# Performance work log

Measured on AMD Instinct MI355X. Metric: run time of the kernel, lower is better.

The kernel has to match this reference:

```python
import jax, jax.numpy as jnp
import numpy as np

REFRACTORY_PERIOD = 5
DAMPENING_FACTOR = 0.3


def setup_inputs() -> dict:
    key = jax.random.key(0)
    B, T, N = 32, 4096, 256
    x = jax.random.normal(key, (B, T, N), dtype=jnp.float32)
    return {"x": x}


def _refractory_scan(x):
    # x: [B, T, N]; scan over time keeping refractory counter q resident.
    B, T, N = x.shape
    xt = jnp.swapaxes(x, 0, 1)  # [T, B, N]

    def step(q, x_t):
        cond = (x_t > 0) & (q == 0)
        z_t = jnp.where(cond, jnp.ones_like(q), jnp.zeros_like(q))
        q = jnp.maximum(jnp.zeros_like(q), q - 1) + REFRACTORY_PERIOD * z_t
        return q, z_t

    q0 = jnp.zeros((B, N), dtype=x.dtype)
    # Note: the t=0 case in the original (z0 = x0>0, q = R*z0) is exactly the
    # first step of this scan starting from q0 = 0.
    _, z = jax.lax.scan(step, q0, xt)
    return jnp.swapaxes(z, 0, 1)  # [B, T, N]


def reference(x) -> jnp.ndarray:
    # Forward value is exactly z_forward (the surrogate-gradient straight-through
    # construction leaves the value unchanged).
    return _refractory_scan(x)
```

## Files before the change

### kernel.cpp

```cpp
#include <hip/hip_runtime.h>
#include <cstdint>
#include <cstddef>

#define BB 32
#define TT 4096
#define NNV 64
#define CC 128
#define PSUB 4
#define PG 8
#define MSG_WORDS 32

__global__ __launch_bounds__(256) void refrac_fused(const float* __restrict__ x,
                                                    float* __restrict__ z,
                                                    uint32_t* __restrict__ msg) {
    const int tid = threadIdx.x;
    const int pg = blockIdx.x >> 5;
    const int b  = blockIdx.x & 31;
    const int psub = tid >> 6;
    const int n4 = tid & 63;
    const int p = pg * PSUB + psub;

    const float4* __restrict__ xv = reinterpret_cast<const float4*>(x)
        + ((size_t)b * TT + (size_t)p * CC) * NNV + n4;

    int na[4][6];
    #pragma unroll
    for (int c = 0; c < 4; ++c)
        #pragma unroll
        for (int e = 0; e < 6; ++e) na[c][e] = e;

    uint32_t bits[4][4];

    #pragma unroll
    for (int w = 0; w < 4; ++w) {
        uint32_t cur[4] = {0u, 0u, 0u, 0u};
        for (int jb = 0; jb < 32; jb += 8) {
            float4 buf[8];
            #pragma unroll
            for (int u = 0; u < 8; ++u)
                buf[u] = xv[(size_t)(w * 32 + jb + u) * NNV];
            #pragma unroll
            for (int u = 0; u < 8; ++u) {
                const int j2 = jb + u;
                const int j  = w * 32 + j2;
                const float4 v = buf[u];
                const float fv[4] = {v.x, v.y, v.z, v.w};
                #pragma unroll
                for (int c = 0; c < 4; ++c) {
                    const bool pos = fv[c] > 0.0f;
                    cur[c] |= pos ? (1u << j2) : 0u;
                    #pragma unroll
                    for (int e = 0; e < 6; ++e)
                        if (pos & (j >= na[c][e])) na[c][e] = j + 6;
                }
            }
        }
        #pragma unroll
        for (int c = 0; c < 4; ++c) bits[c][w] = cur[c];
    }

    __shared__ uint32_t tbl_lds[PSUB][256];
    __shared__ uint8_t  ent_lds[PSUB][256];
    __shared__ uint8_t  sout_lds[256];

    #pragma unroll
    for (int c = 0; c < 4; ++c) {
        uint32_t tbl = 0;
        #pragma unroll
        for (int e = 0; e < 6; ++e) {
            int q = na[c][e] - CC;
            q = q > 0 ? q : 0;
            tbl |= (uint32_t)q << (4 * e);
        }
        tbl_lds[psub][n4 * 4 + c] = tbl;
    }
    __syncthreads();

    {
        const int n = tid;
        int e = 0;
        if (pg > 0) {
            const uint32_t* inw = msg + ((size_t)b * PG + (pg - 1)) * MSG_WORDS + (n >> 3);
            uint32_t wv;
            while ((wv = __hip_atomic_load(inw, __ATOMIC_RELAXED,
                                           __HIP_MEMORY_SCOPE_AGENT)) & 0x88888888u)
                __builtin_amdgcn_s_sleep(1);
            e = (int)((wv >> ((n & 7) * 4)) & 0xFu);
        }
        #pragma unroll
        for (int s = 0; s < PSUB; ++s) {
            ent_lds[s][n] = (uint8_t)e;
            e = (int)((tbl_lds[s][n] >> (4 * e)) & 0xFu);
        }
        sout_lds[n] = (uint8_t)e;
    }
    __syncthreads();

    if (pg < PG - 1 && tid < MSG_WORDS) {
        uint32_t wv = 0;
        #pragma unroll
        for (int k = 0; k < 8; ++k)
            wv |= (uint32_t)sout_lds[tid * 8 + k] << (4 * k);
        __hip_atomic_store(msg + ((size_t)b * PG + pg) * MSG_WORDS + tid, wv,
                           __ATOMIC_RELAXED, __HIP_MEMORY_SCOPE_AGENT);
    }

    float4* __restrict__ zv = reinterpret_cast<float4*>(z)
        + ((size_t)b * TT + (size_t)p * CC) * NNV + n4;

    int ea[4];
    #pragma unroll
    for (int c = 0; c < 4; ++c) ea[c] = (int)ent_lds[psub][n4 * 4 + c];

    #pragma unroll
    for (int w = 0; w < 4; ++w) {
        const uint32_t bw[4] = {bits[0][w], bits[1][w], bits[2][w], bits[3][w]};
        for (int j2 = 0; j2 < 32; ++j2) {
            const int j = w * 32 + j2;
            float o[4];
            #pragma unroll
            for (int c = 0; c < 4; ++c) {
                const bool sp = (((bw[c] >> j2) & 1u) != 0u) & (j >= ea[c]);
                if (sp) ea[c] = j + 6;
                o[c] = sp ? 1.0f : 0.0f;
            }
            zv[(size_t)j * NNV] = make_float4(o[0], o[1], o[2], o[3]);
        }
    }
}

extern "C" void kernel_launch(void* const* d_in, const int* in_sizes, int n_in,
                              void* d_out, int out_size, void* d_ws, size_t ws_size,
                              hipStream_t stream) {
    const float* x = (const float*)d_in[0];
    float* z = (float*)d_out;
    uint32_t* msg = (uint32_t*)d_ws;

    hipMemsetAsync(d_ws, 0xAA, (size_t)BB * PG * MSG_WORDS * sizeof(uint32_t), stream);

    refrac_fused<<<dim3(BB * PG), 256, 0, stream>>>(x, z, msg);
}
```

Measured before the change: 245.7 us.

## Split neuron dimension into two halves to double block count

Each block now handles half of the 256 neurons (2 per thread via float2 instead of 4 via float4), doubling the grid from 256 to 512 blocks. The inter-block chain messages are split per half, so each half's time-chunk chain runs independently. This is meant to raise occupancy and parallelism on a GPU with many CUs, and it halves the per-thread register state. The cost is narrower 8-byte memory accesses, and half the threads sit idle during the cross-chunk table-composition step.

```diff
diff --git a/kernel.cpp b/kernel.cpp
--- a/kernel.cpp
+++ b/kernel.cpp
@@ -4,49 +4,51 @@
 
 #define BB 32
 #define TT 4096
-#define NNV 64
+#define NN 256
 #define CC 128
 #define PSUB 4
 #define PG 8
-#define MSG_WORDS 32
+#define NH 2
+#define HC 128
+#define MSG_WORDS 16
 
 __global__ __launch_bounds__(256) void refrac_fused(const float* __restrict__ x,
                                                     float* __restrict__ z,
                                                     uint32_t* __restrict__ msg) {
-    const int tid = threadIdx.x;
-    const int pg = blockIdx.x >> 5;
-    const int b  = blockIdx.x & 31;
+    const int tid  = threadIdx.x;
+    const int half = blockIdx.x & 1;
+    const int b    = (blockIdx.x >> 1) & 31;
+    const int pg   = blockIdx.x >> 6;
     const int psub = tid >> 6;
-    const int n4 = tid & 63;
-    const int p = pg * PSUB + psub;
+    const int n8   = tid & 63;
+    const int p    = pg * PSUB + psub;
 
-    const float4* __restrict__ xv = reinterpret_cast<const float4*>(x)
-        + ((size_t)b * TT + (size_t)p * CC) * NNV + n4;
+    const float2* __restrict__ xv = reinterpret_cast<const float2*>(
+        x + ((size_t)b * TT + (size_t)p * CC) * NN + half * HC) + n8;
 
-    int na[4][6];
+    int na[2][6];
     #pragma unroll
-    for (int c = 0; c < 4; ++c)
+    for (int c = 0; c < 2; ++c)
         #pragma unroll
         for (int e = 0; e < 6; ++e) na[c][e] = e;
 
-    uint32_t bits[4][4];
+    uint32_t bits[2][4];
 
     #pragma unroll
     for (int w = 0; w < 4; ++w) {
-        uint32_t cur[4] = {0u, 0u, 0u, 0u};
+        uint32_t cur[2] = {0u, 0u};
         for (int jb = 0; jb < 32; jb += 8) {
-            float4 buf[8];
+            float2 buf[8];
             #pragma unroll
             for (int u = 0; u < 8; ++u)
-                buf[u] = xv[(size_t)(w * 32 + jb + u) * NNV];
+                buf[u] = xv[(size_t)(w * 32 + jb + u) * (NN / 2)];
             #pragma unroll
             for (int u = 0; u < 8; ++u) {
                 const int j2 = jb + u;
                 const int j  = w * 32 + j2;
-                const float4 v = buf[u];
-                const float fv[4] = {v.x, v.y, v.z, v.w};
+                const float fv[2] = {buf[u].x, buf[u].y};
                 #pragma unroll
-                for (int c = 0; c < 4; ++c) {
+                for (int c = 0; c < 2; ++c) {
                     const bool pos = fv[c] > 0.0f;
                     cur[c] |= pos ? (1u << j2) : 0u;
                     #pragma unroll
@@ -56,15 +58,15 @@
             }
         }
         #pragma unroll
-        for (int c = 0; c < 4; ++c) bits[c][w] = cur[c];
+        for (int c = 0; c < 2; ++c) bits[c][w] = cur[c];
     }
 
-    __shared__ uint32_t tbl_lds[PSUB][256];
-    __shared__ uint8_t  ent_lds[PSUB][256];
-    __shared__ uint8_t  sout_lds[256];
+    __shared__ uint32_t tbl_lds[PSUB][HC];
+    __shared__ uint8_t  ent_lds[PSUB][HC];
+    __shared__ uint8_t  sout_lds[HC];
 
     #pragma unroll
-    for (int c = 0; c < 4; ++c) {
+    for (int c = 0; c < 2; ++c) {
         uint32_t tbl = 0;
         #pragma unroll
         for (int e = 0; e < 6; ++e) {
@@ -72,15 +74,16 @@
             q = q > 0 ? q : 0;
             tbl |= (uint32_t)q << (4 * e);
         }
-        tbl_lds[psub][n4 * 4 + c] = tbl;
+        tbl_lds[psub][n8 * 2 + c] = tbl;
     }
     __syncthreads();
 
-    {
+    if (tid < HC) {
         const int n = tid;
         int e = 0;
         if (pg > 0) {
-            const uint32_t* inw = msg + ((size_t)b * PG + (pg - 1)) * MSG_WORDS + (n >> 3);
+            const uint32_t* inw = msg +
+                (((size_t)b * PG + (pg - 1)) * NH + half) * MSG_WORDS + (n >> 3);
             uint32_t wv;
             while ((wv = __hip_atomic_load(inw, __ATOMIC_RELAXED,
                                            __HIP_MEMORY_SCOPE_AGENT)) & 0x88888888u)
@@ -101,30 +104,30 @@
         #pragma unroll
         for (int k = 0; k < 8; ++k)
             wv |= (uint32_t)sout_lds[tid * 8 + k] << (4 * k);
-        __hip_atomic_store(msg + ((size_t)b * PG + pg) * MSG_WORDS + tid, wv,
-                           __ATOMIC_RELAXED, __HIP_MEMORY_SCOPE_AGENT);
+        __hip_atomic_store(msg + (((size_t)b * PG + pg) * NH + half) * MSG_WORDS + tid,
+                           wv, __ATOMIC_RELAXED, __HIP_MEMORY_SCOPE_AGENT);
     }
 
-    float4* __restrict__ zv = reinterpret_cast<float4*>(z)
-        + ((size_t)b * TT + (size_t)p * CC) * NNV + n4;
+    float2* __restrict__ zv = reinterpret_cast<float2*>(
+        z + ((size_t)b * TT + (size_t)p * CC) * NN + half * HC) + n8;
 
-    int ea[4];
+    int ea[2];
     #pragma unroll
-    for (int c = 0; c < 4; ++c) ea[c] = (int)ent_lds[psub][n4 * 4 + c];
+    for (int c = 0; c < 2; ++c) ea[c] = (int)ent_lds[psub][n8 * 2 + c];
 
     #pragma unroll
     for (int w = 0; w < 4; ++w) {
-        const uint32_t bw[4] = {bits[0][w], bits[1][w], bits[2][w], bits[3][w]};
+        const uint32_t bw[2] = {bits[0][w], bits[1][w]};
         for (int j2 = 0; j2 < 32; ++j2) {
             const int j = w * 32 + j2;
-            float o[4];
+            float o[2];
             #pragma unroll
-            for (int c = 0; c < 4; ++c) {
+            for (int c = 0; c < 2; ++c) {
                 const bool sp = (((bw[c] >> j2) & 1u) != 0u) & (j >= ea[c]);
                 if (sp) ea[c] = j + 6;
                 o[c] = sp ? 1.0f : 0.0f;
             }
-            zv[(size_t)j * NNV] = make_float4(o[0], o[1], o[2], o[3]);
+            zv[(size_t)j * (NN / 2)] = make_float2(o[0], o[1]);
         }
     }
 }
@@ -136,7 +139,8 @@
     float* z = (float*)d_out;
     uint32_t* msg = (uint32_t*)d_ws;
 
-    hipMemsetAsync(d_ws, 0xAA, (size_t)BB * PG * MSG_WORDS * sizeof(uint32_t), stream);
+    hipMemsetAsync(d_ws, 0xAA,
+                   (size_t)BB * PG * NH * MSG_WORDS * sizeof(uint32_t), stream);
 
-    refrac_fused<<<dim3(BB * PG), 256, 0, stream>>>(x, z, msg);
+    refrac_fused<<<dim3(BB * PG * NH), 256, 0, stream>>>(x, z, msg);
 }
```

After: 279.8 us. +13.9%, slower.

## Split fused decoupled-lookback kernel into scan and emit kernels via global tables

Applied to the files above, without the earlier changes.

Replaces the single fused kernel, in which each chunk group spin-waited on its predecessor's refractory state message, with two kernels. The first computes the per-chunk transition tables and spike bitmasks and writes them to workspace. The second recomposes the chunk-entry states by walking all preceding tables redundantly in each block, then emits the output. This removes the serial inter-block wait chain and the memset, at the cost of an extra launch, workspace round-trip traffic and redundant table loads.

```diff
diff --git a/kernel.cpp b/kernel.cpp
--- a/kernel.cpp
+++ b/kernel.cpp
@@ -4,15 +4,16 @@
 
 #define BB 32
 #define TT 4096
+#define NN 256
 #define NNV 64
 #define CC 128
 #define PSUB 4
+#define PP 32
 #define PG 8
-#define MSG_WORDS 32
 
-__global__ __launch_bounds__(256) void refrac_fused(const float* __restrict__ x,
-                                                    float* __restrict__ z,
-                                                    uint32_t* __restrict__ msg) {
+__global__ __launch_bounds__(256) void refrac_scan(const float* __restrict__ x,
+                                                   uint32_t* __restrict__ tbl,
+                                                   uint32_t* __restrict__ bits_g) {
     const int tid = threadIdx.x;
     const int pg = blockIdx.x >> 5;
     const int b  = blockIdx.x & 31;
@@ -59,68 +60,83 @@
         for (int c = 0; c < 4; ++c) bits[c][w] = cur[c];
     }
 
-    __shared__ uint32_t tbl_lds[PSUB][256];
-    __shared__ uint8_t  ent_lds[PSUB][256];
-    __shared__ uint8_t  sout_lds[256];
+    const size_t row = (size_t)b * PP + p;
 
+    uint32_t t4[4];
     #pragma unroll
     for (int c = 0; c < 4; ++c) {
-        uint32_t tbl = 0;
+        uint32_t t = 0;
         #pragma unroll
         for (int e = 0; e < 6; ++e) {
             int q = na[c][e] - CC;
             q = q > 0 ? q : 0;
-            tbl |= (uint32_t)q << (4 * e);
+            t |= (uint32_t)q << (4 * e);
         }
-        tbl_lds[psub][n4 * 4 + c] = tbl;
+        t4[c] = t;
+    }
+    reinterpret_cast<uint4*>(tbl)[row * NNV + n4] =
+        make_uint4(t4[0], t4[1], t4[2], t4[3]);
+
+    #pragma unroll
+    for (int w = 0; w < 4; ++w)
+        reinterpret_cast<uint4*>(bits_g)[(row * 4 + w) * NNV + n4] =
+            make_uint4(bits[0][w], bits[1][w], bits[2][w], bits[3][w]);
+}
+
+__global__ __launch_bounds__(256) void refrac_emit(const uint32_t* __restrict__ tbl,
+                                                   const uint32_t* __restrict__ bits_g,
+                                                   float* __restrict__ z) {
+    const int tid = threadIdx.x;
+    const int pg = blockIdx.x >> 5;
+    const int b  = blockIdx.x & 31;
+    const int psub = tid >> 6;
+    const int n4 = tid & 63;
+    const int p = pg * PSUB + psub;
+    const int pbase = pg * PSUB;
+
+    __shared__ uint8_t ent_lds[PSUB][NN];
+
+    {
+        const int n = tid;
+        uint32_t tv[PP];
+        #pragma unroll
+        for (int p2 = 0; p2 < PP; ++p2)
+            tv[p2] = (p2 < pbase + PSUB - 1)
+                         ? tbl[((size_t)b * PP + p2) * NN + n] : 0u;
+        int e = 0;
+        #pragma unroll
+        for (int p2 = 0; p2 < PP; ++p2) {
+            if (p2 >= pbase && p2 < pbase + PSUB)
+                ent_lds[p2 - pbase][n] = (uint8_t)e;
+            e = (int)((tv[p2] >> (4 * e)) & 0xFu);
+        }
     }
     __syncthreads();
 
-    {
-        const int n = tid;
-        int e = 0;
-        if (pg > 0) {
-            const uint32_t* inw = msg + ((size_t)b * PG + (pg - 1)) * MSG_WORDS + (n >> 3);
-            uint32_t wv;
-            while ((wv = __hip_atomic_load(inw, __ATOMIC_RELAXED,
-                                           __HIP_MEMORY_SCOPE_AGENT)) & 0x88888888u)
-                __builtin_amdgcn_s_sleep(1);
-            e = (int)((wv >> ((n & 7) * 4)) & 0xFu);
-        }
-        #pragma unroll
-        for (int s = 0; s < PSUB; ++s) {
-            ent_lds[s][n] = (uint8_t)e;
-            e = (int)((tbl_lds[s][n] >> (4 * e)) & 0xFu);
-        }
-        sout_lds[n] = (uint8_t)e;
+    const size_t row = (size_t)b * PP + p;
+    uint32_t bw[4][4];
+    #pragma unroll
+    for (int w = 0; w < 4; ++w) {
+        const uint4 bv =
+            reinterpret_cast<const uint4*>(bits_g)[(row * 4 + w) * NNV + n4];
+        bw[w][0] = bv.x; bw[w][1] = bv.y; bw[w][2] = bv.z; bw[w][3] = bv.w;
     }
-    __syncthreads();
-
-    if (pg < PG - 1 && tid < MSG_WORDS) {
-        uint32_t wv = 0;
-        #pragma unroll
-        for (int k = 0; k < 8; ++k)
-            wv |= (uint32_t)sout_lds[tid * 8 + k] << (4 * k);
-        __hip_atomic_store(msg + ((size_t)b * PG + pg) * MSG_WORDS + tid, wv,
-                           __ATOMIC_RELAXED, __HIP_MEMORY_SCOPE_AGENT);
-    }
-
-    float4* __restrict__ zv = reinterpret_cast<float4*>(z)
-        + ((size_t)b * TT + (size_t)p * CC) * NNV + n4;
 
     int ea[4];
     #pragma unroll
     for (int c = 0; c < 4; ++c) ea[c] = (int)ent_lds[psub][n4 * 4 + c];
 
+    float4* __restrict__ zv = reinterpret_cast<float4*>(z)
+        + ((size_t)b * TT + (size_t)p * CC) * NNV + n4;
+
     #pragma unroll
     for (int w = 0; w < 4; ++w) {
-        const uint32_t bw[4] = {bits[0][w], bits[1][w], bits[2][w], bits[3][w]};
         for (int j2 = 0; j2 < 32; ++j2) {
             const int j = w * 32 + j2;
             float o[4];
             #pragma unroll
             for (int c = 0; c < 4; ++c) {
-                const bool sp = (((bw[c] >> j2) & 1u) != 0u) & (j >= ea[c]);
+                const bool sp = (((bw[w][c] >> j2) & 1u) != 0u) & (j >= ea[c]);
                 if (sp) ea[c] = j + 6;
                 o[c] = sp ? 1.0f : 0.0f;
             }
@@ -134,9 +150,10 @@
                               hipStream_t stream) {
     const float* x = (const float*)d_in[0];
     float* z = (float*)d_out;
-    uint32_t* msg = (uint32_t*)d_ws;
 
-    hipMemsetAsync(d_ws, 0xAA, (size_t)BB * PG * MSG_WORDS * sizeof(uint32_t), stream);
+    uint32_t* tbl = (uint32_t*)d_ws;
+    uint32_t* bits_g = (uint32_t*)((char*)d_ws + (size_t)BB * PP * NN * sizeof(uint32_t));
 
-    refrac_fused<<<dim3(BB * PG), 256, 0, stream>>>(x, z, msg);
+    refrac_scan<<<dim3(BB * PG), 256, 0, stream>>>(x, tbl, bits_g);
+    refrac_emit<<<dim3(BB * PG), 256, 0, stream>>>(tbl, bits_g, z);
 }
```

New measurement: 250.9 us. 1.02x slower.
